# Kernel tuning notes

Hardware: AMD Instinct MI355X
Metric: run time of the kernel (lower is better)

The kernel has to match this reference:

```python
import jax, jax.numpy as jnp
import numpy as np

D_MODEL = 512
DEPTH = 2
D_STATE = 16
D_CONV = 4
EXPAND = 2
D_INNER = EXPAND * D_MODEL
DT_RANK = (D_MODEL + 15) // 16  # ceil(d_model/16) = 32
B_SZ = 8
SEQ = 2048


def setup_inputs() -> dict:
    key = jax.random.key(0)
    ks = jax.random.split(key, 8)
    s = 0.02
    A0 = jnp.log(jnp.broadcast_to(jnp.arange(1, D_STATE + 1, dtype=jnp.float32),
                                  (DEPTH, D_INNER, D_STATE)))
    return {
        "x": jax.random.normal(ks[0], (B_SZ, SEQ, D_MODEL), jnp.float32),
        "ln_w": jnp.ones((DEPTH, D_MODEL), jnp.float32),
        "ln_b": jnp.zeros((DEPTH, D_MODEL), jnp.float32),
        "in_proj_w": jax.random.normal(ks[1], (DEPTH, 2 * D_INNER, D_MODEL), jnp.float32) * s,
        "conv_w": jax.random.normal(ks[2], (DEPTH, D_INNER, 1, D_CONV), jnp.float32) * s,
        "conv_b": jnp.zeros((DEPTH, D_INNER), jnp.float32),
        "x_proj_w": jax.random.normal(ks[3], (DEPTH, DT_RANK + 2 * D_STATE, D_INNER), jnp.float32) * s,
        "dt_proj_w": jax.random.normal(ks[4], (DEPTH, D_INNER, DT_RANK), jnp.float32) * s,
        "dt_proj_b": jax.random.uniform(ks[5], (DEPTH, D_INNER), jnp.float32, -4.0, -2.0),
        "A_log": A0,
        "D_param": jnp.ones((DEPTH, D_INNER), jnp.float32),
        "out_proj_w": jax.random.normal(ks[6], (DEPTH, D_MODEL, D_INNER), jnp.float32) * s,
    }


def _layer_norm(x, w, b):
    mu = x.mean(-1, keepdims=True)
    var = ((x - mu) ** 2).mean(-1, keepdims=True)
    return (x - mu) * jax.lax.rsqrt(var + 1e-5) * w + b


def _mamba_block(x, in_w, cw, cb, xp_w, dtw, dtb, A_log, Dp, ow):
    B = x.shape[0]
    # input projection -> x branch and gate z
    xz = jnp.einsum('bld,ed->ble', x, in_w)          # [B,L,2*d_inner]
    xi, z = jnp.split(xz, 2, axis=-1)
    # depthwise causal conv1d over time
    xc = jnp.transpose(xi, (0, 2, 1))                 # [B,d_inner,L]
    xc = jax.lax.conv_general_dilated(
        xc, cw, (1,), [(D_CONV - 1, 0)],
        dimension_numbers=('NCH', 'OIH', 'NCH'),
        feature_group_count=D_INNER)
    xc = xc + cb[None, :, None]
    xi = jax.nn.silu(jnp.transpose(xc, (0, 2, 1)))    # [B,L,d_inner]
    # input-dependent dt, B, C
    dbc = jnp.einsum('ble,fe->blf', xi, xp_w)         # [B,L,dt_rank+2*d_state]
    dt = dbc[..., :DT_RANK]
    Bm = dbc[..., DT_RANK:DT_RANK + D_STATE]
    Cm = dbc[..., DT_RANK + D_STATE:]
    delta = jax.nn.softplus(jnp.einsum('blr,er->ble', dt, dtw) + dtb)  # [B,L,d_inner]
    A = -jnp.exp(A_log)                               # [d_inner,d_state]

    def step(h, ins):
        d_t, B_t, C_t, u_t = ins                      # [B,E],[B,N],[B,N],[B,E]
        dA = jnp.exp(d_t[..., None] * A)              # [B,E,N]
        h = dA * h + (d_t * u_t)[..., None] * B_t[:, None, :]
        y = jnp.einsum('ben,bn->be', h, C_t)
        return h, y

    h0 = jnp.zeros((B, D_INNER, D_STATE), x.dtype)
    ins = (jnp.transpose(delta, (1, 0, 2)),
           jnp.transpose(Bm, (1, 0, 2)),
           jnp.transpose(Cm, (1, 0, 2)),
           jnp.transpose(xi, (1, 0, 2)))
    _, ys = jax.lax.scan(step, h0, ins)               # ys: [L,B,d_inner]
    y = jnp.transpose(ys, (1, 0, 2)) + xi * Dp        # skip term D*u
    y = y * jax.nn.silu(z)                            # gate
    return jnp.einsum('ble,de->bld', y, ow)           # out projection


def reference(x, ln_w, ln_b, in_proj_w, conv_w, conv_b, x_proj_w,
              dt_proj_w, dt_proj_b, A_log, D_param, out_proj_w):
    for i in range(DEPTH):
        x = x + _mamba_block(_layer_norm(x, ln_w[i], ln_b[i]),
                             in_proj_w[i], conv_w[i], conv_b[i], x_proj_w[i],
                             dt_proj_w[i], dt_proj_b[i], A_log[i], D_param[i],
                             out_proj_w[i])
    return x
```

## Files before the change

kernel.cpp:

```cpp
#include <hip/hip_runtime.h>
#include <hip/hip_bf16.h>
#include <math.h>

#define B_SZ   8
#define SEQ    2048
#define DMODEL 512
#define DEPTH  2
#define DSTATE 16
#define DCONV  4
#define DINNER 1024
#define DTRANK 32
#define ROWS   (B_SZ * SEQ)
#define DBCW   (DTRANK + 2 * DSTATE)

typedef unsigned short u16;
typedef float f32x4 __attribute__((ext_vector_type(4)));
typedef short bf16x8 __attribute__((ext_vector_type(8)));

__device__ __forceinline__ float silu_f(float v) {
    return v * __builtin_amdgcn_rcpf(1.f + __expf(-v));
}
__device__ __forceinline__ float softplus_f(float s) {
    return (s > 20.f) ? s : __logf(1.f + __expf(s));
}
__device__ __forceinline__ u16 f2b(float v) {
    __hip_bfloat16 h = __float2bfloat16(v);
    return *(u16*)&h;
}
__device__ __forceinline__ float b2f(u16 v) {
    __hip_bfloat16 h;
    *(u16*)&h = v;
    return __bfloat162float(h);
}
__device__ __forceinline__ float sum16(float x) {
    x += __int_as_float(__builtin_amdgcn_update_dpp(0, __float_as_int(x), 0x121, 0xf, 0xf, true));
    x += __int_as_float(__builtin_amdgcn_update_dpp(0, __float_as_int(x), 0x122, 0xf, 0xf, true));
    x += __int_as_float(__builtin_amdgcn_update_dpp(0, __float_as_int(x), 0x124, 0xf, 0xf, true));
    x += __int_as_float(__builtin_amdgcn_update_dpp(0, __float_as_int(x), 0x128, 0xf, 0xf, true));
    return x;
}

__device__ __forceinline__ void load_lds16(const void* g, void* l) {
    __builtin_amdgcn_global_load_lds(
        (const __attribute__((address_space(1))) unsigned int*)g,
        (__attribute__((address_space(3))) unsigned int*)l, 16, 0, 0);
}

__global__ __launch_bounds__(256) void f2bf(const float* __restrict__ in,
                                            __hip_bfloat16* __restrict__ out, int n) {
    int i = blockIdx.x * 256 + threadIdx.x;
    if (i < n) out[i] = __float2bfloat16(in[i]);
}

__global__ __launch_bounds__(256) void ln_kernel(const float* __restrict__ x,
                                                 const float* __restrict__ w,
                                                 const float* __restrict__ b,
                                                 __hip_bfloat16* __restrict__ out) {
    int r = blockIdx.x;
    int tid = threadIdx.x;
    const float* xr = x + (size_t)r * DMODEL;
    float2 v = *(const float2*)(xr + tid * 2);
    float s = v.x + v.y;
    float s2 = v.x * v.x + v.y * v.y;
    #pragma unroll
    for (int off = 1; off < 64; off <<= 1) {
        s  += __shfl_xor(s, off);
        s2 += __shfl_xor(s2, off);
    }
    __shared__ float ws[4], ws2[4];
    int wid = tid >> 6, lane = tid & 63;
    if (lane == 0) { ws[wid] = s; ws2[wid] = s2; }
    __syncthreads();
    float ts = ws[0] + ws[1] + ws[2] + ws[3];
    float ts2 = ws2[0] + ws2[1] + ws2[2] + ws2[3];
    float mean = ts * (1.f / DMODEL);
    float var = ts2 * (1.f / DMODEL) - mean * mean;
    float inv = rsqrtf(var + 1e-5f);
    out[(size_t)r * DMODEL + tid * 2]     = __float2bfloat16((v.x - mean) * inv * w[tid * 2] + b[tid * 2]);
    out[(size_t)r * DMODEL + tid * 2 + 1] = __float2bfloat16((v.y - mean) * inv * w[tid * 2 + 1] + b[tid * 2 + 1]);
}

template <bool RES>
__global__ __launch_bounds__(256) void gemm_bf16(const u16* __restrict__ A, int lda,
                                                 const u16* __restrict__ W,
                                                 const float* __restrict__ res,
                                                 float* __restrict__ C,
                                                 int M, int N, int K) {
    __shared__ u16 As[128 * 32];
    __shared__ u16 Bs[128 * 32];
    int tid = threadIdx.x;
    int wave = tid >> 6, lane = tid & 63;
    int wm = (wave >> 1) * 64, wn = (wave & 1) * 64;
    int m0 = blockIdx.y * 128, n0 = blockIdx.x * 128;
    int srow = lane >> 2, sseg = lane & 3;
    const u16* Ag = A + (size_t)(m0 + wave * 32 + srow) * lda + sseg * 8;
    const u16* Wg = W + (size_t)(n0 + wave * 32 + srow) * K + sseg * 8;
    u16* Asw = As + wave * 32 * 32;
    u16* Bsw = Bs + wave * 32 * 32;

    f32x4 acc[4][4] = {};
    int col = lane & 15, quad = lane >> 4;

    for (int k0 = 0; k0 < K; k0 += 32) {
        __syncthreads();
        load_lds16(Ag + k0, Asw);
        load_lds16(Ag + k0 + (size_t)16 * lda, Asw + 16 * 32);
        load_lds16(Wg + k0, Bsw);
        load_lds16(Wg + k0 + (size_t)16 * K, Bsw + 16 * 32);
        __syncthreads();
        bf16x8 af[4], bfr[4];
        #pragma unroll
        for (int i = 0; i < 4; ++i) {
            af[i]  = *(const bf16x8*)(As + (wm + i * 16 + col) * 32 + quad * 8);
            bfr[i] = *(const bf16x8*)(Bs + (wn + i * 16 + col) * 32 + quad * 8);
        }
        #pragma unroll
        for (int i = 0; i < 4; ++i)
            #pragma unroll
            for (int j = 0; j < 4; ++j)
                acc[i][j] = __builtin_amdgcn_mfma_f32_16x16x32_bf16(af[i], bfr[j], acc[i][j], 0, 0, 0);
    }
    #pragma unroll
    for (int i = 0; i < 4; ++i) {
        int gm_base = m0 + wm + i * 16 + quad * 4;
        #pragma unroll
        for (int j = 0; j < 4; ++j) {
            int gn = n0 + wn + j * 16 + col;
            #pragma unroll
            for (int r = 0; r < 4; ++r) {
                size_t off = (size_t)(gm_base + r) * N + gn;
                float v = acc[i][j][r];
                if (RES) v += res[off];
                C[off] = v;
            }
        }
    }
}

__global__ __launch_bounds__(256) void gemm_xp_bf16(const u16* __restrict__ A,
                                                    const u16* __restrict__ W,
                                                    float* __restrict__ C) {
    __shared__ u16 As[128 * 32];
    __shared__ u16 Bs[64 * 32];
    int tid = threadIdx.x;
    int wave = tid >> 6, lane = tid & 63;
    int m0 = blockIdx.x * 128;
    int wm = wave * 32;
    int srow = lane >> 2, sseg = lane & 3;
    const u16* Ag = A + (size_t)(m0 + wm + srow) * DINNER + sseg * 8;
    const u16* Wg = W + (size_t)(wave * 16 + srow) * DINNER + sseg * 8;
    u16* Asw = As + wave * 32 * 32;
    u16* Bsw = Bs + wave * 16 * 32;

    f32x4 acc[2][4] = {};
    int col = lane & 15, quad = lane >> 4;

    for (int k0 = 0; k0 < DINNER; k0 += 32) {
        __syncthreads();
        load_lds16(Ag + k0, Asw);
        load_lds16(Ag + k0 + (size_t)16 * DINNER, Asw + 16 * 32);
        load_lds16(Wg + k0, Bsw);
        __syncthreads();
        bf16x8 af[2], bfr[4];
        #pragma unroll
        for (int i = 0; i < 2; ++i)
            af[i] = *(const bf16x8*)(As + (wm + i * 16 + col) * 32 + quad * 8);
        #pragma unroll
        for (int j = 0; j < 4; ++j)
            bfr[j] = *(const bf16x8*)(Bs + (j * 16 + col) * 32 + quad * 8);
        #pragma unroll
        for (int i = 0; i < 2; ++i)
            #pragma unroll
            for (int j = 0; j < 4; ++j)
                acc[i][j] = __builtin_amdgcn_mfma_f32_16x16x32_bf16(af[i], bfr[j], acc[i][j], 0, 0, 0);
    }
    #pragma unroll
    for (int i = 0; i < 2; ++i) {
        int gm_base = m0 + wm + i * 16 + quad * 4;
        #pragma unroll
        for (int j = 0; j < 4; ++j) {
            int gn = j * 16 + col;
            #pragma unroll
            for (int r = 0; r < 4; ++r)
                C[(size_t)(gm_base + r) * DBCW + gn] = acc[i][j][r];
        }
    }
}

__global__ __launch_bounds__(256) void u_t_kernel(const float* __restrict__ xz,
                                                  const float* __restrict__ cw,
                                                  const float* __restrict__ cb,
                                                  u16* __restrict__ ut,
                                                  u16* __restrict__ u_re) {
    __shared__ float xt[67][65];
    __shared__ u16 uo[64][70];
    int tid = threadIdx.x;
    int t0 = blockIdx.x * 64, e0 = blockIdx.y * 64, b = blockIdx.z;
    int er = tid & 63, rr = tid >> 6;
    for (int it = 0; it < 17; ++it) {
        int row = it * 4 + rr;
        if (row < 67) {
            int t = t0 + row - 3;
            xt[row][er] = (t >= 0) ? xz[((size_t)b * SEQ + t) * (2 * DINNER) + e0 + er] : 0.f;
        }
    }
    __syncthreads();
    {
        int e = tid & 63, tg = tid >> 6;
        float4 w4 = *(const float4*)(cw + (e0 + e) * 4);
        float cbe = cb[e0 + e];
        int tl0 = tg * 16;
        float x3 = xt[tl0][e], x2 = xt[tl0 + 1][e], x1 = xt[tl0 + 2][e];
        #pragma unroll
        for (int i = 0; i < 16; ++i) {
            float x0 = xt[tl0 + i + 3][e];
            float u = silu_f(cbe + w4.x * x3 + w4.y * x2 + w4.z * x1 + w4.w * x0);
            x3 = x2; x2 = x1; x1 = x0;
            u16 ub = f2b(u);
            uo[e][tl0 + i] = ub;
            u_re[((size_t)b * SEQ + t0 + tl0 + i) * DINNER + e0 + e] = ub;
        }
    }
    __syncthreads();
    {
        int tl = tid & 63, eg = tid >> 6;
        #pragma unroll
        for (int i = 0; i < 16; ++i) {
            int ee = eg * 16 + i;
            ut[((size_t)b * DINNER + e0 + ee) * SEQ + t0 + tl] = uo[ee][tl];
        }
    }
}

__global__ __launch_bounds__(256) void delta_t_kernel(const float* __restrict__ dbc,
                                                      const float* __restrict__ dtw,
                                                      const float* __restrict__ dtb,
                                                      u16* __restrict__ dlt) {
    __shared__ float wl[64 * 32];
    __shared__ float bl[64];
    int tid = threadIdx.x;
    int e0 = blockIdx.x * 64, t0 = blockIdx.y * 256, b = blockIdx.z;
    for (int i = tid; i < 64 * 32; i += 256) wl[i] = dtw[(size_t)e0 * DTRANK + i];
    if (tid < 64) bl[tid] = dtb[e0 + tid];
    float dreg[32];
    const float* dp = dbc + (size_t)(b * SEQ + t0 + tid) * DBCW;
    #pragma unroll
    for (int k = 0; k < 32; k += 4) {
        float4 v = *(const float4*)(dp + k);
        dreg[k] = v.x; dreg[k + 1] = v.y; dreg[k + 2] = v.z; dreg[k + 3] = v.w;
    }
    __syncthreads();
    for (int ep = 0; ep < 64; ++ep) {
        float s = bl[ep];
        #pragma unroll
        for (int k = 0; k < 32; ++k) s += dreg[k] * wl[ep * 32 + k];
        dlt[((size_t)b * DINNER + e0 + ep) * SEQ + t0 + tid] = f2b(softplus_f(s));
    }
}

__global__ __launch_bounds__(256) void bct_kernel(const float* __restrict__ dbc,
                                                  u16* __restrict__ Bt, u16* __restrict__ Ct) {
    int tid = threadIdx.x;
    int t = blockIdx.x * 256 + tid, b = blockIdx.y;
    const float* dp = dbc + (size_t)(b * SEQ + t) * DBCW + DTRANK;
    #pragma unroll
    for (int n = 0; n < DSTATE; ++n)
        Bt[((size_t)b * DSTATE + n) * SEQ + t] = f2b(dp[n]);
    #pragma unroll
    for (int n = 0; n < DSTATE; ++n)
        Ct[((size_t)b * DSTATE + n) * SEQ + t] = f2b(dp[DSTATE + n]);
}

#define SCHUNK 8

__global__ __launch_bounds__(256, 2) void scan_fused(float* xz,
                                                     const u16* __restrict__ ut,
                                                     const u16* __restrict__ dlt,
                                                     const u16* __restrict__ Bt,
                                                     const u16* __restrict__ Ct,
                                                     const float* __restrict__ Alog,
                                                     const float* __restrict__ Dp) {
    int tid = threadIdx.x;
    int pair = tid >> 4, n = tid & 15;
    int blk = blockIdx.x;
    int b = blk >> 6;
    int e = ((blk & 63) << 4) + pair;
    float a = -__expf(Alog[e * DSTATE + n]);
    float dpe = Dp[e];
    const u16* urow  = ut  + ((size_t)b * DINNER + e) * SEQ;
    const u16* dlrow = dlt + ((size_t)b * DINNER + e) * SEQ;
    const u16* Brow  = Bt + ((size_t)b * DSTATE + n) * SEQ;
    const u16* Crow  = Ct + ((size_t)b * DSTATE + n) * SEQ;
    float* yrow = xz + (size_t)b * SEQ * (2 * DINNER) + e;

    float h = 0.f;
    bf16x8 Au, Adl, AB, AC, Bu, Bdl, BB, BC, Cu, Cdl, CB, CC, Du, Ddl, DB, DC;

    auto load = [&](int c, bf16x8& u8, bf16x8& d8, bf16x8& b8, bf16x8& c8) {
        u8 = *(const bf16x8*)(urow + c * SCHUNK);
        d8 = *(const bf16x8*)(dlrow + c * SCHUNK);
        b8 = *(const bf16x8*)(Brow + c * SCHUNK);
        c8 = *(const bf16x8*)(Crow + c * SCHUNK);
    };
    auto proc = [&](int c, bf16x8 u8, bf16x8 d8, bf16x8 b8, bf16x8 c8) {
        float* yp_ = yrow + (size_t)c * SCHUNK * (2 * DINNER);
        #pragma unroll
        for (int j = 0; j < SCHUNK; ++j) {
            float uf = b2f((u16)u8[j]);
            float dl = b2f((u16)d8[j]);
            float dA = __expf(dl * a);
            h = dA * h + (dl * uf) * b2f((u16)b8[j]);
            float yp = sum16(h * b2f((u16)c8[j]));
            if (n == 0) yp_[(size_t)j * (2 * DINNER)] = yp + uf * dpe;
        }
    };

    const int nc = SEQ / SCHUNK;
    load(0, Au, Adl, AB, AC);
    load(1, Bu, Bdl, BB, BC);
    for (int c = 0; c < nc; c += 4) {
        if (c + 2 < nc) load(c + 2, Cu, Cdl, CB, CC);
        if (c + 3 < nc) load(c + 3, Du, Ddl, DB, DC);
        proc(c, Au, Adl, AB, AC);
        proc(c + 1, Bu, Bdl, BB, BC);
        if (c + 4 < nc) load(c + 4, Au, Adl, AB, AC);
        if (c + 5 < nc) load(c + 5, Bu, Bdl, BB, BC);
        proc(c + 2, Cu, Cdl, CB, CC);
        proc(c + 3, Du, Ddl, DB, DC);
    }
}

__global__ __launch_bounds__(256) void gate_pack(float* xz) {
    int r = blockIdx.x, tid = threadIdx.x;
    float* row = xz + (size_t)r * (2 * DINNER);
    float4 yr = ((const float4*)row)[tid];
    float4 zz = ((const float4*)(row + DINNER))[tid];
    __syncthreads();
    ushort4 o;
    o.x = f2b(yr.x * silu_f(zz.x));
    o.y = f2b(yr.y * silu_f(zz.y));
    o.z = f2b(yr.z * silu_f(zz.z));
    o.w = f2b(yr.w * silu_f(zz.w));
    ((ushort4*)row)[tid] = o;
}

extern "C" void kernel_launch(void* const* d_in, const int* in_sizes, int n_in,
                              void* d_out, int out_size, void* d_ws, size_t ws_size,
                              hipStream_t stream) {
    const float* x_in   = (const float*)d_in[0];
    const float* ln_w   = (const float*)d_in[1];
    const float* ln_b   = (const float*)d_in[2];
    const float* inw    = (const float*)d_in[3];
    const float* convw  = (const float*)d_in[4];
    const float* convb  = (const float*)d_in[5];
    const float* xpw    = (const float*)d_in[6];
    const float* dtw    = (const float*)d_in[7];
    const float* dtb    = (const float*)d_in[8];
    const float* Alog   = (const float*)d_in[9];
    const float* Dp     = (const float*)d_in[10];
    const float* outw   = (const float*)d_in[11];
    float* out = (float*)d_out;

    char* p = (char*)d_ws;
    float* xz  = (float*)p;                 p += (size_t)ROWS * 2 * DINNER * 4;
    float* dbc = (float*)p;                 p += (size_t)ROWS * DBCW * 4;
    u16*   dlt = (u16*)p;                   p += (size_t)B_SZ * DINNER * SEQ * 2;
    u16*   u_re = dlt;
    u16*   Bt  = (u16*)p;                   p += (size_t)B_SZ * DSTATE * SEQ * 2;
    u16*   Ct  = (u16*)p;                   p += (size_t)B_SZ * DSTATE * SEQ * 2;
    u16*   ut  = (u16*)p;                   p += (size_t)B_SZ * DINNER * SEQ * 2;
    __hip_bfloat16* xnbf = (__hip_bfloat16*)ut;
    __hip_bfloat16* inwbf  = (__hip_bfloat16*)p;  p += (size_t)2 * DINNER * DMODEL * 2;
    u16* xwbf = (u16*)inwbf;
    __hip_bfloat16* outwbf = (__hip_bfloat16*)p;  p += (size_t)DMODEL * DINNER * 2;

    const dim3 blk256(256);
    const int n_inw  = 2 * DINNER * DMODEL;
    const int n_outw = DMODEL * DINNER;
    const int n_xw   = DBCW * DINNER;

    for (int i = 0; i < DEPTH; ++i) {
        const float* x_cur = (i == 0) ? x_in : out;
        const float* lw  = ln_w  + (size_t)i * DMODEL;
        const float* lb  = ln_b  + (size_t)i * DMODEL;
        const float* iw  = inw   + (size_t)i * 2 * DINNER * DMODEL;
        const float* cw  = convw + (size_t)i * DINNER * DCONV;
        const float* cb  = convb + (size_t)i * DINNER;
        const float* xw  = xpw   + (size_t)i * DBCW * DINNER;
        const float* dw  = dtw   + (size_t)i * DINNER * DTRANK;
        const float* db  = dtb   + (size_t)i * DINNER;
        const float* Al  = Alog  + (size_t)i * DINNER * DSTATE;
        const float* Dpp = Dp    + (size_t)i * DINNER;
        const float* ow  = outw  + (size_t)i * DMODEL * DINNER;

        f2bf<<<(n_inw + 255) / 256, blk256, 0, stream>>>(iw, inwbf, n_inw);
        f2bf<<<(n_outw + 255) / 256, blk256, 0, stream>>>(ow, outwbf, n_outw);
        ln_kernel<<<ROWS, blk256, 0, stream>>>(x_cur, lw, lb, xnbf);
        gemm_bf16<false><<<dim3(2 * DINNER / 128, ROWS / 128), blk256, 0, stream>>>(
            (const u16*)xnbf, DMODEL, (const u16*)inwbf, nullptr, xz, ROWS, 2 * DINNER, DMODEL);
        f2bf<<<(n_xw + 255) / 256, blk256, 0, stream>>>(xw, (__hip_bfloat16*)xwbf, n_xw);
        u_t_kernel<<<dim3(SEQ / 64, DINNER / 64, B_SZ), blk256, 0, stream>>>(xz, cw, cb, ut, u_re);
        gemm_xp_bf16<<<ROWS / 128, blk256, 0, stream>>>(u_re, xwbf, dbc);
        delta_t_kernel<<<dim3(DINNER / 64, SEQ / 256, B_SZ), blk256, 0, stream>>>(dbc, dw, db, dlt);
        bct_kernel<<<dim3(SEQ / 256, B_SZ), blk256, 0, stream>>>(dbc, Bt, Ct);
        scan_fused<<<(B_SZ * DINNER) / 16, blk256, 0, stream>>>(
            xz, ut, dlt, Bt, Ct, Al, Dpp);
        gate_pack<<<ROWS, blk256, 0, stream>>>(xz);
        gemm_bf16<true><<<dim3(DMODEL / 128, ROWS / 128), blk256, 0, stream>>>(
            (const u16*)xz, 2 * DINNER * 2, (const u16*)outwbf, x_cur, out, ROWS, DMODEL, DINNER);
    }
}
```

Before: 1.055 ms.

## Split selective scan into two time halves with carry fixup pass

Splits the sequential scan into two independent halves over time, each run by its own block, which doubles the number of blocks in flight and halves the serial chain length. The second half starts from zero state. A cumsum kernel builds prefix sums of delta, and a fixup kernel adds the contribution of the first half's final state, decayed by exp(A * cumulative delta), to the outputs. The bct kernel is also folded into the delta kernel. The cost is extra launches, an extra read-modify-write over half of y, and reuse of workspace (dbc for carry, ut for St) that depends on those buffers being dead at that point.

```diff
diff --git a/kernel.cpp b/kernel.cpp
--- a/kernel.cpp
+++ b/kernel.cpp
@@ -232,10 +232,12 @@
     }
 }
 
-__global__ __launch_bounds__(256) void delta_t_kernel(const float* __restrict__ dbc,
-                                                      const float* __restrict__ dtw,
-                                                      const float* __restrict__ dtb,
-                                                      u16* __restrict__ dlt) {
+__global__ __launch_bounds__(256) void delta_bct_kernel(const float* __restrict__ dbc,
+                                                        const float* __restrict__ dtw,
+                                                        const float* __restrict__ dtb,
+                                                        u16* __restrict__ dlt,
+                                                        u16* __restrict__ Bt,
+                                                        u16* __restrict__ Ct) {
     __shared__ float wl[64 * 32];
     __shared__ float bl[64];
     int tid = threadIdx.x;
@@ -256,45 +258,43 @@
         for (int k = 0; k < 32; ++k) s += dreg[k] * wl[ep * 32 + k];
         dlt[((size_t)b * DINNER + e0 + ep) * SEQ + t0 + tid] = f2b(softplus_f(s));
     }
-}
-
-__global__ __launch_bounds__(256) void bct_kernel(const float* __restrict__ dbc,
-                                                  u16* __restrict__ Bt, u16* __restrict__ Ct) {
-    int tid = threadIdx.x;
-    int t = blockIdx.x * 256 + tid, b = blockIdx.y;
-    const float* dp = dbc + (size_t)(b * SEQ + t) * DBCW + DTRANK;
-    #pragma unroll
-    for (int n = 0; n < DSTATE; ++n)
-        Bt[((size_t)b * DSTATE + n) * SEQ + t] = f2b(dp[n]);
-    #pragma unroll
-    for (int n = 0; n < DSTATE; ++n)
-        Ct[((size_t)b * DSTATE + n) * SEQ + t] = f2b(dp[DSTATE + n]);
+    if (blockIdx.x == 0) {
+        int t = t0 + tid;
+        const float* dp2 = dbc + (size_t)(b * SEQ + t) * DBCW + DTRANK;
+        #pragma unroll
+        for (int nn = 0; nn < DSTATE; ++nn) {
+            Bt[((size_t)b * DSTATE + nn) * SEQ + t] = f2b(dp2[nn]);
+            Ct[((size_t)b * DSTATE + nn) * SEQ + t] = f2b(dp2[DSTATE + nn]);
+        }
+    }
 }
 
 #define SCHUNK 8
 
-__global__ __launch_bounds__(256, 2) void scan_fused(float* xz,
-                                                     const u16* __restrict__ ut,
-                                                     const u16* __restrict__ dlt,
-                                                     const u16* __restrict__ Bt,
-                                                     const u16* __restrict__ Ct,
-                                                     const float* __restrict__ Alog,
-                                                     const float* __restrict__ Dp) {
+__global__ __launch_bounds__(256, 4) void scan_half(float* xz,
+                                                    const u16* __restrict__ ut,
+                                                    const u16* __restrict__ dlt,
+                                                    const u16* __restrict__ Bt,
+                                                    const u16* __restrict__ Ct,
+                                                    const float* __restrict__ Alog,
+                                                    const float* __restrict__ Dp,
+                                                    float* __restrict__ carry) {
     int tid = threadIdx.x;
     int pair = tid >> 4, n = tid & 15;
-    int blk = blockIdx.x;
-    int b = blk >> 6;
-    int e = ((blk & 63) << 4) + pair;
+    int pg = blockIdx.x >> 1, half = blockIdx.x & 1;
+    int b = pg >> 6;
+    int e = ((pg & 63) << 4) + pair;
+    int t_off = half << 10;
     float a = -__expf(Alog[e * DSTATE + n]);
     float dpe = Dp[e];
-    const u16* urow  = ut  + ((size_t)b * DINNER + e) * SEQ;
-    const u16* dlrow = dlt + ((size_t)b * DINNER + e) * SEQ;
-    const u16* Brow  = Bt + ((size_t)b * DSTATE + n) * SEQ;
-    const u16* Crow  = Ct + ((size_t)b * DSTATE + n) * SEQ;
-    float* yrow = xz + (size_t)b * SEQ * (2 * DINNER) + e;
+    const u16* urow  = ut  + ((size_t)b * DINNER + e) * SEQ + t_off;
+    const u16* dlrow = dlt + ((size_t)b * DINNER + e) * SEQ + t_off;
+    const u16* Brow  = Bt + ((size_t)b * DSTATE + n) * SEQ + t_off;
+    const u16* Crow  = Ct + ((size_t)b * DSTATE + n) * SEQ + t_off;
+    float* yrow = xz + ((size_t)b * SEQ + t_off) * (2 * DINNER) + e;
 
     float h = 0.f;
-    bf16x8 Au, Adl, AB, AC, Bu, Bdl, BB, BC, Cu, Cdl, CB, CC, Du, Ddl, DB, DC;
+    bf16x8 Au, Adl, AB, AC, Bu, Bdl, BB, BC;
 
     auto load = [&](int c, bf16x8& u8, bf16x8& d8, bf16x8& b8, bf16x8& c8) {
         u8 = *(const bf16x8*)(urow + c * SCHUNK);
@@ -315,18 +315,74 @@
         }
     };
 
-    const int nc = SEQ / SCHUNK;
+    const int nc = 1024 / SCHUNK;
     load(0, Au, Adl, AB, AC);
-    load(1, Bu, Bdl, BB, BC);
-    for (int c = 0; c < nc; c += 4) {
-        if (c + 2 < nc) load(c + 2, Cu, Cdl, CB, CC);
-        if (c + 3 < nc) load(c + 3, Du, Ddl, DB, DC);
+    for (int c = 0; c < nc; c += 2) {
+        load(c + 1, Bu, Bdl, BB, BC);
         proc(c, Au, Adl, AB, AC);
+        if (c + 2 < nc) load(c + 2, Au, Adl, AB, AC);
         proc(c + 1, Bu, Bdl, BB, BC);
-        if (c + 4 < nc) load(c + 4, Au, Adl, AB, AC);
-        if (c + 5 < nc) load(c + 5, Bu, Bdl, BB, BC);
-        proc(c + 2, Cu, Cdl, CB, CC);
-        proc(c + 3, Du, Ddl, DB, DC);
+    }
+    if (half == 0) carry[pg * 256 + tid] = h;
+}
+
+__global__ __launch_bounds__(256) void cumsum_kernel(const u16* __restrict__ dlt,
+                                                     float* __restrict__ St) {
+    int row = blockIdx.x;
+    int tid = threadIdx.x;
+    const u16* dp = dlt + (size_t)row * SEQ + 1024;
+    ushort4 d4 = *(const ushort4*)(dp + tid * 4);
+    float s1 = b2f(d4.x);
+    float s2 = s1 + b2f(d4.y);
+    float s3 = s2 + b2f(d4.z);
+    float s4 = s3 + b2f(d4.w);
+    __shared__ float ts[256];
+    ts[tid] = s4;
+    __syncthreads();
+    float acc = s4;
+    for (int off = 1; off < 256; off <<= 1) {
+        float v = (tid >= off) ? ts[tid - off] : 0.f;
+        __syncthreads();
+        acc += v;
+        ts[tid] = acc;
+        __syncthreads();
+    }
+    float base = acc - s4;
+    float4 o = {base + s1, base + s2, base + s3, base + s4};
+    *(float4*)(St + (size_t)row * 1024 + tid * 4) = o;
+}
+
+__global__ __launch_bounds__(256, 4) void fixup_kernel(float* xz,
+                                                       const u16* __restrict__ Ct,
+                                                       const float* __restrict__ St,
+                                                       const float* __restrict__ carry,
+                                                       const float* __restrict__ Alog) {
+    int tid = threadIdx.x;
+    int pair = tid >> 4, n = tid & 15;
+    int pg = blockIdx.x >> 3, tc = blockIdx.x & 7;
+    int b = pg >> 6;
+    int e = ((pg & 63) << 4) + pair;
+    float a = -__expf(Alog[e * DSTATE + n]);
+    float h0 = carry[pg * 256 + tid];
+    const u16* Crow = Ct + ((size_t)b * DSTATE + n) * SEQ + 1024 + tc * 128;
+    const float* Srow = St + ((size_t)b * DINNER + e) * 1024 + tc * 128;
+    float* yrow = xz + ((size_t)b * SEQ + 1024 + tc * 128) * (2 * DINNER) + e;
+
+    for (int c = 0; c < 16; ++c) {
+        bf16x8 C8 = *(const bf16x8*)(Crow + c * 8);
+        float4 Sa = *(const float4*)(Srow + c * 8);
+        float4 Sb = *(const float4*)(Srow + c * 8 + 4);
+        float Sv[8] = {Sa.x, Sa.y, Sa.z, Sa.w, Sb.x, Sb.y, Sb.z, Sb.w};
+        float* yp = yrow + (size_t)c * 8 * (2 * DINNER);
+        #pragma unroll
+        for (int j = 0; j < 8; ++j) {
+            float g = __expf(a * Sv[j]) * h0;
+            float corr = sum16(g * b2f((u16)C8[j]));
+            if (n == 0) {
+                float* addr = yp + (size_t)j * (2 * DINNER);
+                *addr = *addr + corr;
+            }
+        }
     }
 }
 
@@ -364,12 +420,14 @@
     char* p = (char*)d_ws;
     float* xz  = (float*)p;                 p += (size_t)ROWS * 2 * DINNER * 4;
     float* dbc = (float*)p;                 p += (size_t)ROWS * DBCW * 4;
+    float* carry = dbc;
     u16*   dlt = (u16*)p;                   p += (size_t)B_SZ * DINNER * SEQ * 2;
     u16*   u_re = dlt;
     u16*   Bt  = (u16*)p;                   p += (size_t)B_SZ * DSTATE * SEQ * 2;
     u16*   Ct  = (u16*)p;                   p += (size_t)B_SZ * DSTATE * SEQ * 2;
     u16*   ut  = (u16*)p;                   p += (size_t)B_SZ * DINNER * SEQ * 2;
     __hip_bfloat16* xnbf = (__hip_bfloat16*)ut;
+    float* St = (float*)ut;
     __hip_bfloat16* inwbf  = (__hip_bfloat16*)p;  p += (size_t)2 * DINNER * DMODEL * 2;
     u16* xwbf = (u16*)inwbf;
     __hip_bfloat16* outwbf = (__hip_bfloat16*)p;  p += (size_t)DMODEL * DINNER * 2;
@@ -401,10 +459,13 @@
         f2bf<<<(n_xw + 255) / 256, blk256, 0, stream>>>(xw, (__hip_bfloat16*)xwbf, n_xw);
         u_t_kernel<<<dim3(SEQ / 64, DINNER / 64, B_SZ), blk256, 0, stream>>>(xz, cw, cb, ut, u_re);
         gemm_xp_bf16<<<ROWS / 128, blk256, 0, stream>>>(u_re, xwbf, dbc);
-        delta_t_kernel<<<dim3(DINNER / 64, SEQ / 256, B_SZ), blk256, 0, stream>>>(dbc, dw, db, dlt);
-        bct_kernel<<<dim3(SEQ / 256, B_SZ), blk256, 0, stream>>>(dbc, Bt, Ct);
-        scan_fused<<<(B_SZ * DINNER) / 16, blk256, 0, stream>>>(
-            xz, ut, dlt, Bt, Ct, Al, Dpp);
+        delta_bct_kernel<<<dim3(DINNER / 64, SEQ / 256, B_SZ), blk256, 0, stream>>>(
+            dbc, dw, db, dlt, Bt, Ct);
+        scan_half<<<(B_SZ * DINNER) / 16 * 2, blk256, 0, stream>>>(
+            xz, ut, dlt, Bt, Ct, Al, Dpp, carry);
+        cumsum_kernel<<<B_SZ * DINNER, blk256, 0, stream>>>(dlt, St);
+        fixup_kernel<<<(B_SZ * DINNER) / 16 * 8, blk256, 0, stream>>>(
+            xz, Ct, St, carry, Al);
         gate_pack<<<ROWS, blk256, 0, stream>>>(xz);
         gemm_bf16<true><<<dim3(DMODEL / 128, ROWS / 128), blk256, 0, stream>>>(
             (const u16*)xz, 2 * DINNER * 2, (const u16*)outwbf, x_cur, out, ROWS, DMODEL, DINNER);
```

Result: slower. 1.245 ms (+18.0%).

## Store projections in bf16, fuse SiLU gate into GEMM and scan, merge small kernels

Applied to the files above, without the earlier changes.

The input-projection GEMM now writes x and silu(z) as separate bf16 buffers instead of one fp32 xz buffer. The z gate is transposed together with u and multiplied inside the scan, so the scan emits gated bf16 y directly and the gate_pack pass disappears. The three weight conversions are merged into one launch, the B/C transpose is folded into the delta kernel, and the scan prefetch depth drops from four chunks to two. The goal is less HBM traffic and fewer launches; in exchange the scan reads an extra stream and more intermediates are held at bf16 precision.

```diff
diff --git a/kernel.cpp b/kernel.cpp
--- a/kernel.cpp
+++ b/kernel.cpp
@@ -46,16 +46,25 @@
         (__attribute__((address_space(3))) unsigned int*)l, 16, 0, 0);
 }
 
-__global__ __launch_bounds__(256) void f2bf(const float* __restrict__ in,
-                                            __hip_bfloat16* __restrict__ out, int n) {
+#define N_INW  (2 * DINNER * DMODEL)
+#define N_OUTW (DMODEL * DINNER)
+#define N_XW   (DBCW * DINNER)
+__global__ __launch_bounds__(256) void conv_weights(const float* __restrict__ iw,
+                                                    const float* __restrict__ ow,
+                                                    const float* __restrict__ xw,
+                                                    u16* __restrict__ inwbf,
+                                                    u16* __restrict__ outwbf,
+                                                    u16* __restrict__ xwbf) {
     int i = blockIdx.x * 256 + threadIdx.x;
-    if (i < n) out[i] = __float2bfloat16(in[i]);
+    if (i < N_INW) inwbf[i] = f2b(iw[i]);
+    else if (i < N_INW + N_OUTW) outwbf[i - N_INW] = f2b(ow[i - N_INW]);
+    else if (i < N_INW + N_OUTW + N_XW) xwbf[i - N_INW - N_OUTW] = f2b(xw[i - N_INW - N_OUTW]);
 }
 
 __global__ __launch_bounds__(256) void ln_kernel(const float* __restrict__ x,
                                                  const float* __restrict__ w,
                                                  const float* __restrict__ b,
-                                                 __hip_bfloat16* __restrict__ out) {
+                                                 u16* __restrict__ out) {
     int r = blockIdx.x;
     int tid = threadIdx.x;
     const float* xr = x + (size_t)r * DMODEL;
@@ -76,24 +85,23 @@
     float mean = ts * (1.f / DMODEL);
     float var = ts2 * (1.f / DMODEL) - mean * mean;
     float inv = rsqrtf(var + 1e-5f);
-    out[(size_t)r * DMODEL + tid * 2]     = __float2bfloat16((v.x - mean) * inv * w[tid * 2] + b[tid * 2]);
-    out[(size_t)r * DMODEL + tid * 2 + 1] = __float2bfloat16((v.y - mean) * inv * w[tid * 2 + 1] + b[tid * 2 + 1]);
-}
-
-template <bool RES>
-__global__ __launch_bounds__(256) void gemm_bf16(const u16* __restrict__ A, int lda,
-                                                 const u16* __restrict__ W,
-                                                 const float* __restrict__ res,
-                                                 float* __restrict__ C,
-                                                 int M, int N, int K) {
+    out[(size_t)r * DMODEL + tid * 2]     = f2b((v.x - mean) * inv * w[tid * 2] + b[tid * 2]);
+    out[(size_t)r * DMODEL + tid * 2 + 1] = f2b((v.y - mean) * inv * w[tid * 2 + 1] + b[tid * 2 + 1]);
+}
+
+__global__ __launch_bounds__(256) void gemm_in(const u16* __restrict__ A,
+                                               const u16* __restrict__ W,
+                                               u16* __restrict__ xi_re,
+                                               u16* __restrict__ sz_re) {
     __shared__ u16 As[128 * 32];
     __shared__ u16 Bs[128 * 32];
+    const int K = DMODEL, N = 2 * DINNER;
     int tid = threadIdx.x;
     int wave = tid >> 6, lane = tid & 63;
     int wm = (wave >> 1) * 64, wn = (wave & 1) * 64;
     int m0 = blockIdx.y * 128, n0 = blockIdx.x * 128;
     int srow = lane >> 2, sseg = lane & 3;
-    const u16* Ag = A + (size_t)(m0 + wave * 32 + srow) * lda + sseg * 8;
+    const u16* Ag = A + (size_t)(m0 + wave * 32 + srow) * K + sseg * 8;
     const u16* Wg = W + (size_t)(n0 + wave * 32 + srow) * K + sseg * 8;
     u16* Asw = As + wave * 32 * 32;
     u16* Bsw = Bs + wave * 32 * 32;
@@ -104,7 +112,7 @@
     for (int k0 = 0; k0 < K; k0 += 32) {
         __syncthreads();
         load_lds16(Ag + k0, Asw);
-        load_lds16(Ag + k0 + (size_t)16 * lda, Asw + 16 * 32);
+        load_lds16(Ag + k0 + (size_t)16 * K, Asw + 16 * 32);
         load_lds16(Wg + k0, Bsw);
         load_lds16(Wg + k0 + (size_t)16 * K, Bsw + 16 * 32);
         __syncthreads();
@@ -120,18 +128,74 @@
             for (int j = 0; j < 4; ++j)
                 acc[i][j] = __builtin_amdgcn_mfma_f32_16x16x32_bf16(af[i], bfr[j], acc[i][j], 0, 0, 0);
     }
+    bool is_z = (n0 >= DINNER);
+    u16* dst = is_z ? sz_re : xi_re;
+    int nb = n0 & (DINNER - 1);
     #pragma unroll
     for (int i = 0; i < 4; ++i) {
         int gm_base = m0 + wm + i * 16 + quad * 4;
         #pragma unroll
         for (int j = 0; j < 4; ++j) {
+            int gn = nb + wn + j * 16 + col;
+            #pragma unroll
+            for (int r = 0; r < 4; ++r) {
+                float v = acc[i][j][r];
+                if (is_z) v = silu_f(v);
+                dst[(size_t)(gm_base + r) * DINNER + gn] = f2b(v);
+            }
+        }
+    }
+}
+
+__global__ __launch_bounds__(256) void gemm_out(const u16* __restrict__ A,
+                                                const u16* __restrict__ W,
+                                                const float* __restrict__ res,
+                                                float* __restrict__ C) {
+    __shared__ u16 As[128 * 32];
+    __shared__ u16 Bs[128 * 32];
+    const int K = DINNER, N = DMODEL;
+    int tid = threadIdx.x;
+    int wave = tid >> 6, lane = tid & 63;
+    int wm = (wave >> 1) * 64, wn = (wave & 1) * 64;
+    int m0 = blockIdx.y * 128, n0 = blockIdx.x * 128;
+    int srow = lane >> 2, sseg = lane & 3;
+    const u16* Ag = A + (size_t)(m0 + wave * 32 + srow) * K + sseg * 8;
+    const u16* Wg = W + (size_t)(n0 + wave * 32 + srow) * K + sseg * 8;
+    u16* Asw = As + wave * 32 * 32;
+    u16* Bsw = Bs + wave * 32 * 32;
+
+    f32x4 acc[4][4] = {};
+    int col = lane & 15, quad = lane >> 4;
+
+    for (int k0 = 0; k0 < K; k0 += 32) {
+        __syncthreads();
+        load_lds16(Ag + k0, Asw);
+        load_lds16(Ag + k0 + (size_t)16 * K, Asw + 16 * 32);
+        load_lds16(Wg + k0, Bsw);
+        load_lds16(Wg + k0 + (size_t)16 * K, Bsw + 16 * 32);
+        __syncthreads();
+        bf16x8 af[4], bfr[4];
+        #pragma unroll
+        for (int i = 0; i < 4; ++i) {
+            af[i]  = *(const bf16x8*)(As + (wm + i * 16 + col) * 32 + quad * 8);
+            bfr[i] = *(const bf16x8*)(Bs + (wn + i * 16 + col) * 32 + quad * 8);
+        }
+        #pragma unroll
+        for (int i = 0; i < 4; ++i)
+            #pragma unroll
+            for (int j = 0; j < 4; ++j)
+                acc[i][j] = __builtin_amdgcn_mfma_f32_16x16x32_bf16(af[i], bfr[j], acc[i][j], 0, 0, 0);
+    }
+    #pragma unroll
+    for (int i = 0; i < 4; ++i) {
+        int gm_base = m0 + wm + i * 16 + quad * 4;
+        #pragma unroll
+        for (int j = 0; j < 4; ++j) {
             int gn = n0 + wn + j * 16 + col;
             #pragma unroll
             for (int r = 0; r < 4; ++r) {
                 size_t off = (size_t)(gm_base + r) * N + gn;
-                float v = acc[i][j][r];
-                if (RES) v += res[off];
-                C[off] = v;
+                C[off] = acc[i][j][r] + res[off];
             }
         }
     }
@@ -187,13 +251,16 @@
     }
 }
 
-__global__ __launch_bounds__(256) void u_t_kernel(const float* __restrict__ xz,
+__global__ __launch_bounds__(256) void u_t_kernel(const u16* __restrict__ xi_re,
+                                                  const u16* __restrict__ sz_re,
                                                   const float* __restrict__ cw,
                                                   const float* __restrict__ cb,
                                                   u16* __restrict__ ut,
-                                                  u16* __restrict__ u_re) {
+                                                  u16* __restrict__ u_re,
+                                                  u16* __restrict__ szt) {
     __shared__ float xt[67][65];
     __shared__ u16 uo[64][70];
+    __shared__ u16 szo[64][70];
     int tid = threadIdx.x;
     int t0 = blockIdx.x * 64, e0 = blockIdx.y * 64, b = blockIdx.z;
     int er = tid & 63, rr = tid >> 6;
@@ -201,8 +268,13 @@
         int row = it * 4 + rr;
         if (row < 67) {
             int t = t0 + row - 3;
-            xt[row][er] = (t >= 0) ? xz[((size_t)b * SEQ + t) * (2 * DINNER) + e0 + er] : 0.f;
-        }
+            xt[row][er] = (t >= 0) ? b2f(xi_re[((size_t)b * SEQ + t) * DINNER + e0 + er]) : 0.f;
+        }
+    }
+    #pragma unroll
+    for (int it = 0; it < 16; ++it) {
+        int row = it * 4 + rr;
+        szo[er][row] = sz_re[((size_t)b * SEQ + t0 + row) * DINNER + e0 + er];
     }
     __syncthreads();
     {
@@ -228,14 +300,17 @@
         for (int i = 0; i < 16; ++i) {
             int ee = eg * 16 + i;
             ut[((size_t)b * DINNER + e0 + ee) * SEQ + t0 + tl] = uo[ee][tl];
-        }
-    }
-}
-
-__global__ __launch_bounds__(256) void delta_t_kernel(const float* __restrict__ dbc,
-                                                      const float* __restrict__ dtw,
-                                                      const float* __restrict__ dtb,
-                                                      u16* __restrict__ dlt) {
+            szt[((size_t)b * DINNER + e0 + ee) * SEQ + t0 + tl] = szo[ee][tl];
+        }
+    }
+}
+
+__global__ __launch_bounds__(256) void delta_bct_kernel(const float* __restrict__ dbc,
+                                                        const float* __restrict__ dtw,
+                                                        const float* __restrict__ dtb,
+                                                        u16* __restrict__ dlt,
+                                                        u16* __restrict__ Bt,
+                                                        u16* __restrict__ Ct) {
     __shared__ float wl[64 * 32];
     __shared__ float bl[64];
     int tid = threadIdx.x;
@@ -256,28 +331,25 @@
         for (int k = 0; k < 32; ++k) s += dreg[k] * wl[ep * 32 + k];
         dlt[((size_t)b * DINNER + e0 + ep) * SEQ + t0 + tid] = f2b(softplus_f(s));
     }
-}
-
-__global__ __launch_bounds__(256) void bct_kernel(const float* __restrict__ dbc,
-                                                  u16* __restrict__ Bt, u16* __restrict__ Ct) {
-    int tid = threadIdx.x;
-    int t = blockIdx.x * 256 + tid, b = blockIdx.y;
-    const float* dp = dbc + (size_t)(b * SEQ + t) * DBCW + DTRANK;
-    #pragma unroll
-    for (int n = 0; n < DSTATE; ++n)
-        Bt[((size_t)b * DSTATE + n) * SEQ + t] = f2b(dp[n]);
-    #pragma unroll
-    for (int n = 0; n < DSTATE; ++n)
-        Ct[((size_t)b * DSTATE + n) * SEQ + t] = f2b(dp[DSTATE + n]);
+    if (blockIdx.x == 0) {
+        int t = t0 + tid;
+        const float* dp2 = dbc + (size_t)(b * SEQ + t) * DBCW + DTRANK;
+        #pragma unroll
+        for (int nn = 0; nn < DSTATE; ++nn) {
+            Bt[((size_t)b * DSTATE + nn) * SEQ + t] = f2b(dp2[nn]);
+            Ct[((size_t)b * DSTATE + nn) * SEQ + t] = f2b(dp2[DSTATE + nn]);
+        }
+    }
 }
 
 #define SCHUNK 8
 
-__global__ __launch_bounds__(256, 2) void scan_fused(float* xz,
+__global__ __launch_bounds__(256, 2) void scan_fused(u16* __restrict__ y_re,
                                                      const u16* __restrict__ ut,
                                                      const u16* __restrict__ dlt,
                                                      const u16* __restrict__ Bt,
                                                      const u16* __restrict__ Ct,
+                                                     const u16* __restrict__ szt,
                                                      const float* __restrict__ Alog,
                                                      const float* __restrict__ Dp) {
     int tid = threadIdx.x;
@@ -289,21 +361,23 @@
     float dpe = Dp[e];
     const u16* urow  = ut  + ((size_t)b * DINNER + e) * SEQ;
     const u16* dlrow = dlt + ((size_t)b * DINNER + e) * SEQ;
+    const u16* szrow = szt + ((size_t)b * DINNER + e) * SEQ;
     const u16* Brow  = Bt + ((size_t)b * DSTATE + n) * SEQ;
     const u16* Crow  = Ct + ((size_t)b * DSTATE + n) * SEQ;
-    float* yrow = xz + (size_t)b * SEQ * (2 * DINNER) + e;
+    u16* yrow = y_re + (size_t)b * SEQ * DINNER + e;
 
     float h = 0.f;
-    bf16x8 Au, Adl, AB, AC, Bu, Bdl, BB, BC, Cu, Cdl, CB, CC, Du, Ddl, DB, DC;
-
-    auto load = [&](int c, bf16x8& u8, bf16x8& d8, bf16x8& b8, bf16x8& c8) {
+    bf16x8 Au, Adl, AB, AC, Asz, Bu, Bdl, BB, BC, Bsz;
+
+    auto load = [&](int c, bf16x8& u8, bf16x8& d8, bf16x8& b8, bf16x8& c8, bf16x8& s8) {
         u8 = *(const bf16x8*)(urow + c * SCHUNK);
         d8 = *(const bf16x8*)(dlrow + c * SCHUNK);
         b8 = *(const bf16x8*)(Brow + c * SCHUNK);
         c8 = *(const bf16x8*)(Crow + c * SCHUNK);
+        s8 = *(const bf16x8*)(szrow + c * SCHUNK);
     };
-    auto proc = [&](int c, bf16x8 u8, bf16x8 d8, bf16x8 b8, bf16x8 c8) {
-        float* yp_ = yrow + (size_t)c * SCHUNK * (2 * DINNER);
+    auto proc = [&](int c, bf16x8 u8, bf16x8 d8, bf16x8 b8, bf16x8 c8, bf16x8 s8) {
+        u16* yp_ = yrow + (size_t)c * SCHUNK * DINNER;
         #pragma unroll
         for (int j = 0; j < SCHUNK; ++j) {
             float uf = b2f((u16)u8[j]);
@@ -311,37 +385,19 @@
             float dA = __expf(dl * a);
             h = dA * h + (dl * uf) * b2f((u16)b8[j]);
             float yp = sum16(h * b2f((u16)c8[j]));
-            if (n == 0) yp_[(size_t)j * (2 * DINNER)] = yp + uf * dpe;
+            if (n == 0)
+                yp_[(size_t)j * DINNER] = f2b((yp + uf * dpe) * b2f((u16)s8[j]));
         }
     };
 
     const int nc = SEQ / SCHUNK;
-    load(0, Au, Adl, AB, AC);
-    load(1, Bu, Bdl, BB, BC);
-    for (int c = 0; c < nc; c += 4) {
-        if (c + 2 < nc) load(c + 2, Cu, Cdl, CB, CC);
-        if (c + 3 < nc) load(c + 3, Du, Ddl, DB, DC);
-        proc(c, Au, Adl, AB, AC);
-        proc(c + 1, Bu, Bdl, BB, BC);
-        if (c + 4 < nc) load(c + 4, Au, Adl, AB, AC);
-        if (c + 5 < nc) load(c + 5, Bu, Bdl, BB, BC);
-        proc(c + 2, Cu, Cdl, CB, CC);
-        proc(c + 3, Du, Ddl, DB, DC);
-    }
-}
-
-__global__ __launch_bounds__(256) void gate_pack(float* xz) {
-    int r = blockIdx.x, tid = threadIdx.x;
-    float* row = xz + (size_t)r * (2 * DINNER);
-    float4 yr = ((const float4*)row)[tid];
-    float4 zz = ((const float4*)(row + DINNER))[tid];
-    __syncthreads();
-    ushort4 o;
-    o.x = f2b(yr.x * silu_f(zz.x));
-    o.y = f2b(yr.y * silu_f(zz.y));
-    o.z = f2b(yr.z * silu_f(zz.z));
-    o.w = f2b(yr.w * silu_f(zz.w));
-    ((ushort4*)row)[tid] = o;
+    load(0, Au, Adl, AB, AC, Asz);
+    for (int c = 0; c < nc; c += 2) {
+        load(c + 1, Bu, Bdl, BB, BC, Bsz);
+        proc(c, Au, Adl, AB, AC, Asz);
+        if (c + 2 < nc) load(c + 2, Au, Adl, AB, AC, Asz);
+        proc(c + 1, Bu, Bdl, BB, BC, Bsz);
+    }
 }
 
 extern "C" void kernel_launch(void* const* d_in, const int* in_sizes, int n_in,
@@ -362,22 +418,23 @@
     float* out = (float*)d_out;
 
     char* p = (char*)d_ws;
-    float* xz  = (float*)p;                 p += (size_t)ROWS * 2 * DINNER * 4;
-    float* dbc = (float*)p;                 p += (size_t)ROWS * DBCW * 4;
-    u16*   dlt = (u16*)p;                   p += (size_t)B_SZ * DINNER * SEQ * 2;
-    u16*   u_re = dlt;
-    u16*   Bt  = (u16*)p;                   p += (size_t)B_SZ * DSTATE * SEQ * 2;
-    u16*   Ct  = (u16*)p;                   p += (size_t)B_SZ * DSTATE * SEQ * 2;
-    u16*   ut  = (u16*)p;                   p += (size_t)B_SZ * DINNER * SEQ * 2;
-    __hip_bfloat16* xnbf = (__hip_bfloat16*)ut;
-    __hip_bfloat16* inwbf  = (__hip_bfloat16*)p;  p += (size_t)2 * DINNER * DMODEL * 2;
-    u16* xwbf = (u16*)inwbf;
-    __hip_bfloat16* outwbf = (__hip_bfloat16*)p;  p += (size_t)DMODEL * DINNER * 2;
+    u16* xi_re = (u16*)p;               p += (size_t)ROWS * DINNER * 2;
+    u16* sz_re = (u16*)p;               p += (size_t)ROWS * DINNER * 2;
+    u16* y_re  = (u16*)p;               p += (size_t)ROWS * DINNER * 2;
+    float* dbc = (float*)p;             p += (size_t)ROWS * DBCW * 4;
+    u16* dlt   = (u16*)p;               p += (size_t)B_SZ * DINNER * SEQ * 2;
+    u16* u_re  = dlt;
+    u16* Bt    = (u16*)p;               p += (size_t)B_SZ * DSTATE * SEQ * 2;
+    u16* xwbf  = Bt;
+    u16* Ct    = (u16*)p;               p += (size_t)B_SZ * DSTATE * SEQ * 2;
+    u16* ut    = (u16*)p;               p += (size_t)B_SZ * DINNER * SEQ * 2;
+    u16* xnbf  = ut;
+    u16* szt   = (u16*)p;               p += (size_t)B_SZ * DINNER * SEQ * 2;
+    u16* inwbf = (u16*)p;               p += (size_t)N_INW * 2;
+    u16* outwbf = (u16*)p;              p += (size_t)N_OUTW * 2;
 
     const dim3 blk256(256);
-    const int n_inw  = 2 * DINNER * DMODEL;
-    const int n_outw = DMODEL * DINNER;
-    const int n_xw   = DBCW * DINNER;
+    const int n_conv = N_INW + N_OUTW + N_XW;
 
     for (int i = 0; i < DEPTH; ++i) {
         const float* x_cur = (i == 0) ? x_in : out;
@@ -393,20 +450,19 @@
         const float* Dpp = Dp    + (size_t)i * DINNER;
         const float* ow  = outw  + (size_t)i * DMODEL * DINNER;
 
-        f2bf<<<(n_inw + 255) / 256, blk256, 0, stream>>>(iw, inwbf, n_inw);
-        f2bf<<<(n_outw + 255) / 256, blk256, 0, stream>>>(ow, outwbf, n_outw);
+        conv_weights<<<(n_conv + 255) / 256, blk256, 0, stream>>>(
+            iw, ow, xw, inwbf, outwbf, xwbf);
         ln_kernel<<<ROWS, blk256, 0, stream>>>(x_cur, lw, lb, xnbf);
-        gemm_bf16<false><<<dim3(2 * DINNER / 128, ROWS / 128), blk256, 0, stream>>>(
-            (const u16*)xnbf, DMODEL, (const u16*)inwbf, nullptr, xz, ROWS, 2 * DINNER, DMODEL);
-        f2bf<<<(n_xw + 255) / 256, blk256, 0, stream>>>(xw, (__hip_bfloat16*)xwbf, n_xw);
-        u_t_kernel<<<dim3(SEQ / 64, DINNER / 64, B_SZ), blk256, 0, stream>>>(xz, cw, cb, ut, u_re);
+        gemm_in<<<dim3(2 * DINNER / 128, ROWS / 128), blk256, 0, stream>>>(
+            xnbf, inwbf, xi_re, sz_re);
+        u_t_kernel<<<dim3(SEQ / 64, DINNER / 64, B_SZ), blk256, 0, stream>>>(
+            xi_re, sz_re, cw, cb, ut, u_re, szt);
         gemm_xp_bf16<<<ROWS / 128, blk256, 0, stream>>>(u_re, xwbf, dbc);
-        delta_t_kernel<<<dim3(DINNER / 64, SEQ / 256, B_SZ), blk256, 0, stream>>>(dbc, dw, db, dlt);
-        bct_kernel<<<dim3(SEQ / 256, B_SZ), blk256, 0, stream>>>(dbc, Bt, Ct);
+        delta_bct_kernel<<<dim3(DINNER / 64, SEQ / 256, B_SZ), blk256, 0, stream>>>(
+            dbc, dw, db, dlt, Bt, Ct);
         scan_fused<<<(B_SZ * DINNER) / 16, blk256, 0, stream>>>(
-            xz, ut, dlt, Bt, Ct, Al, Dpp);
-        gate_pack<<<ROWS, blk256, 0, stream>>>(xz);
-        gemm_bf16<true><<<dim3(DMODEL / 128, ROWS / 128), blk256, 0, stream>>>(
-            (const u16*)xz, 2 * DINNER * 2, (const u16*)outwbf, x_cur, out, ROWS, DMODEL, DINNER);
-    }
-}
+            y_re, ut, dlt, Bt, Ct, szt, Al, Dpp);
+        gemm_out<<<dim3(DMODEL / 128, ROWS / 128), blk256, 0, stream>>>(
+            y_re, outwbf, x_cur, out);
+    }
+}
```

Measured after the change: 980.0 us. 7.1% less time.
